# Performance work log

Hardware: AMD Instinct MI355X
Metric: run time of the kernel (lower is better)

## Reference

```python
import jax, jax.numpy as jnp
import numpy as np

N, P, C, K = 1024, 64, 64, 16
C_MID, C_OUT = 128, 128


def setup_inputs() -> dict:
    key = jax.random.key(0)
    k1, k2, k3, k4 = jax.random.split(key, 4)
    x = jax.random.normal(k1, (N, P, C), dtype=jnp.float32)
    mask = jnp.zeros((N, P), dtype=bool)  # True = padded particle
    # Conv2d(2C -> C_MID, 1x1, no bias); Conv2d(C_MID -> C_OUT, 1x1, no bias)
    W1 = jax.random.normal(k2, (C_MID, 2 * C), dtype=jnp.float32) * 0.05
    W2 = jax.random.normal(k3, (C_OUT, C_MID), dtype=jnp.float32) * 0.05
    # Conv1d(C -> C_OUT, kernel 1, no bias) residual path
    Wres = jax.random.normal(k4, (C_OUT, C), dtype=jnp.float32) * 0.05
    return {"x": x, "mask": mask, "W1": W1, "W2": W2, "Wres": Wres}


def reference(x, mask, W1, W2, Wres):
    n, p, c = x.shape
    k = K
    # residual: Conv1d kernel-1 == per-particle matmul  (N,P,C)->(N,P,C_OUT)
    x_res = jnp.einsum('npc,oc->npo', x, Wres)
    # direction = x with padded rows set to +inf (mask all False here)
    direction = jnp.where(mask[..., None], jnp.inf, x)
    # pairwise L2 distance over channel dim: (N,P,P)
    diff = direction[:, :, None, :] - direction[:, None, :, :]
    dist = jnp.sqrt(jnp.sum(diff * diff, axis=-1))
    # smallest K+1 distances, drop self
    _, idx = jax.lax.top_k(-dist, k + 1)
    knn = idx[..., 1:]  # (N,P,K)
    # faithful to torch: gather along the CHANNEL dim with particle indices
    f_center = jnp.broadcast_to(x[:, :, None, :], (n, p, k, c))  # (N,P,K,C)
    f_neighbor = jnp.take_along_axis(f_center, knn[..., None], axis=-1)  # (N,P,K,1)
    feat = jnp.concatenate([f_center, f_center - f_neighbor], axis=-1)  # (N,P,K,2C)
    # 1x1 conv MLP (channels-last layout)
    h = jax.nn.relu(jnp.einsum('npkc,oc->npko', feat, W1))
    h = jax.nn.relu(jnp.einsum('npkc,oc->npko', h, W2))  # (N,P,K,C_OUT)
    # mask neighbors pointing at padded slots, masked mean over K
    n_valid = p - jnp.sum(mask, axis=-1)  # (N,)
    mask_K = knn >= n_valid[:, None, None]  # (N,P,K) bool
    h = jnp.where(mask_K[..., None], 0.0, h)
    denom = (k - jnp.sum(mask_K, axis=-1)).astype(h.dtype)  # (N,P)
    agg = jnp.sum(h, axis=2) / denom[..., None]  # (N,P,C_OUT)
    return jax.nn.relu(agg + x_res)
```

## Files before the change

### kernel.cpp

```cpp
#include <hip/hip_runtime.h>
#include <hip/hip_bf16.h>

typedef __bf16 bf16x8 __attribute__((ext_vector_type(8)));
typedef float  f32x4  __attribute__((ext_vector_type(4)));
typedef unsigned long long u64;

#define MFMA_BF16 __builtin_amdgcn_mfma_f32_16x16x32_bf16

#define WS_W2P  (1u << 20)
#define WS_WCP  ((1u << 20) + 32768u)
#define WS_SSUM ((1u << 20) + 65536u)

#define K1_XS   0
#define K1_SD   17408
#define K1_SQ   34048
#define K1_LDS  38144

__global__ __launch_bounds__(256, 3)
void knn_kernel(const float* __restrict__ x, const float* __restrict__ W1,
                const float* __restrict__ W2, const float* __restrict__ Wres,
                unsigned* __restrict__ ws)
{
    __shared__ char smem[K1_LDS];
    float*    xs   = (float*)(smem + K1_XS);
    float*    sd_t = (float*)(smem + K1_SD);
    unsigned* sqp  = (unsigned*)(smem + K1_SQ);

    const int tid = threadIdx.x;
    const int n   = blockIdx.x;
    const float* __restrict__ xn = x + (size_t)n * 4096;

    #pragma unroll
    for (int i = 0; i < 4; ++i) {
        int e4 = tid + 256 * i;
        f32x4 v = *(const f32x4*)(xn + e4 * 4);
        int row = e4 >> 4, col = (e4 & 15) * 4;
        float* dst = xs + row * 68 + col;
        dst[0] = v[0]; dst[1] = v[1]; dst[2] = v[2]; dst[3] = v[3];
    }
    __syncthreads();

    {
#pragma clang fp contract(off)
        const int p = tid >> 2, rb = tid & 3;
        f32x4 xp4[16];
        const f32x4* xprow = (const f32x4*)(xs + p * 68);
        #pragma unroll
        for (int v = 0; v < 16; ++v) xp4[v] = xprow[v];
        u64 keys[16];
        #pragma unroll
        for (int i = 0; i < 16; ++i) {
            const int q = 4 * i + rb;
            const f32x4* xq4 = (const f32x4*)(xs + q * 68);
            f32x4 d0 = xp4[0] - xq4[0];
            f32x4 d1 = xp4[1] - xq4[1];
            f32x4 rA = d0 * d0;
            f32x4 rB = d1 * d1;
            #pragma unroll
            for (int b = 1; b < 8; ++b) {
                f32x4 e0 = xp4[2*b]   - xq4[2*b];   rA = rA + e0 * e0;
                f32x4 e1 = xp4[2*b+1] - xq4[2*b+1]; rB = rB + e1 * e1;
            }
            float d2 = ((rA[0]+rA[1]) + (rA[2]+rA[3])) + ((rB[0]+rB[1]) + (rB[2]+rB[3]));
            float key = sqrtf(d2);
            unsigned kb = __float_as_uint(key);
            if (q == p) kb = 0x7f800000u;
            keys[i] = ((u64)kb << 8) | (unsigned)q;
        }
        #pragma unroll
        for (int pp = 1; pp < 16; pp <<= 1) {
            #pragma unroll
            for (int k = pp; k >= 1; k >>= 1) {
                #pragma unroll
                for (int j = k & (pp - 1); j + k < 16; j += 2 * k) {
                    #pragma unroll
                    for (int i = 0; i < k; ++i) {
                        if (i + j + k < 16 && ((i + j) / (2 * pp) == (i + j + k) / (2 * pp))) {
                            u64 a = keys[i + j], b = keys[i + j + k];
                            u64 lo = a < b ? a : b;
                            u64 hi = a < b ? b : a;
                            keys[i + j] = lo; keys[i + j + k] = hi;
                        }
                    }
                }
            }
        }
        #pragma unroll
        for (int t = 0; t < 4; ++t) {
            unsigned wq = 0;
            #pragma unroll
            for (int b = 0; b < 4; ++b) {
                int s = 4 * t + b;
                sd_t[(rb * 16 + s) * 65 + p] = __uint_as_float((unsigned)(keys[s] >> 8));
                wq |= ((unsigned)(keys[s] & 0x3fu)) << (8 * b);
            }
            sqp[(rb * 4 + t) * 64 + p] = wq;
        }
    }
    __syncthreads();

    if (tid < 64) {
        const int p = tid;
        float dh[4]; unsigned qh[4]; int ix[4];
        #pragma unroll
        for (int b = 0; b < 4; ++b) {
            ix[b] = 0;
            dh[b] = sd_t[(b * 16) * 65 + p];
            qh[b] = sqp[(b * 4) * 64 + p] & 63u;
        }
        unsigned knacc[4] = {0u, 0u, 0u, 0u};
        for (int s = 0; s < 16; ++s) {
            int bsel = 0; float bd = dh[0]; unsigned bq = qh[0];
            #pragma unroll
            for (int b = 1; b < 4; ++b) {
                bool t = (dh[b] < bd) || (dh[b] == bd && qh[b] < bq);
                if (t) { bd = dh[b]; bq = qh[b]; bsel = b; }
            }
            knacc[s >> 2] |= bq << ((s & 3) * 8);
            int ni = ix[bsel] + 1; ix[bsel] = ni;
            int nc = ni < 15 ? ni : 15;
            float nd = sd_t[(bsel * 16 + nc) * 65 + p];
            unsigned nw = sqp[(bsel * 4 + (nc >> 2)) * 64 + p];
            unsigned nq = (nw >> ((nc & 3) * 8)) & 63u;
            if (ni > 15) nd = __builtin_inff();
            dh[bsel] = nd; qh[bsel] = nq;
        }
        *(uint4*)(ws + (size_t)n * 256 + p * 4) =
            make_uint4(knacc[0], knacc[1], knacc[2], knacc[3]);
    }

    if (n < 32) {
        if (tid < 64) {
            const int l = tid, f = n;
            int ntl = f >> 2, kt = f & 3;
            int o = ntl * 16 + (l & 15);
            int c = kt * 32 + (l >> 4) * 8;
            const float* s0 = W2 + o * 128 + c;
            f32x4 a0 = *(const f32x4*)s0, a1 = *(const f32x4*)(s0 + 4);
            bf16x8 fr;
            fr[0]=(__bf16)a0[0]; fr[1]=(__bf16)a0[1]; fr[2]=(__bf16)a0[2]; fr[3]=(__bf16)a0[3];
            fr[4]=(__bf16)a1[0]; fr[5]=(__bf16)a1[1]; fr[6]=(__bf16)a1[2]; fr[7]=(__bf16)a1[3];
            *(bf16x8*)((__bf16*)((char*)ws + WS_W2P) + (size_t)(f * 64 + l) * 8) = fr;
        }
    } else if (n < 64) {
        if (tid < 64) {
            const int l = tid, f = n - 32;
            int wv = f >> 3, rem = f & 7, ntl = rem >> 1, kt = rem & 1;
            int o = wv * 64 + ntl * 16 + (l & 15);
            int c = kt * 32 + (l >> 4) * 8;
            float v[8];
            if (o < 128) {
                const float* s0 = W1 + o * 128 + c;
                f32x4 a0 = *(const f32x4*)s0,      a1 = *(const f32x4*)(s0 + 4);
                f32x4 b0 = *(const f32x4*)(s0+64), b1 = *(const f32x4*)(s0 + 68);
                v[0]=a0[0]+b0[0]; v[1]=a0[1]+b0[1]; v[2]=a0[2]+b0[2]; v[3]=a0[3]+b0[3];
                v[4]=a1[0]+b1[0]; v[5]=a1[1]+b1[1]; v[6]=a1[2]+b1[2]; v[7]=a1[3]+b1[3];
            } else {
                const float* s0 = Wres + (o - 128) * 64 + c;
                f32x4 a0 = *(const f32x4*)s0, a1 = *(const f32x4*)(s0 + 4);
                v[0]=a0[0]; v[1]=a0[1]; v[2]=a0[2]; v[3]=a0[3];
                v[4]=a1[0]; v[5]=a1[1]; v[6]=a1[2]; v[7]=a1[3];
            }
            bf16x8 fr;
            #pragma unroll
            for (int j = 0; j < 8; ++j) fr[j] = (__bf16)v[j];
            *(bf16x8*)((__bf16*)((char*)ws + WS_WCP) + (size_t)(f * 64 + l) * 8) = fr;
        }
    } else if (n == 64) {
        if (tid < 128) {
            const f32x4* src = (const f32x4*)(W1 + tid * 128 + 64);
            f32x4 a = {0.f, 0.f, 0.f, 0.f};
            #pragma unroll
            for (int i = 0; i < 16; ++i) a += src[i];
            ((float*)((char*)ws + WS_SSUM))[tid] = a[0] + a[1] + a[2] + a[3];
        }
    }
}

#define K2_UB   0
#define K2_XR   32768
#define K2_SS   65536
#define K2_LDS  66048

__global__ __launch_bounds__(256, 2)
void gemm_kernel(const float* __restrict__ x, const unsigned* __restrict__ ws,
                 float* __restrict__ out)
{
    __shared__ char smem[K2_LDS];
    __bf16*   ub   = (__bf16*)(smem + K2_UB);
    __bf16*   xres = (__bf16*)(smem + K2_XR);
    float*    Ssum = (float*)(smem + K2_SS);

    const __bf16* __restrict__ w2p   = (const __bf16*)((const char*)ws + WS_W2P);
    const __bf16* __restrict__ wcp   = (const __bf16*)((const char*)ws + WS_WCP);
    const float*  __restrict__ ssums = (const float*)((const char*)ws + WS_SSUM);

    const int tid  = threadIdx.x;
    const int lane = tid & 63;
    const int w    = tid >> 6;
    const int lm   = lane & 15;
    const int lq   = lane >> 4;
    const int n0   = blockIdx.x * 2;

    if (tid < 128) Ssum[tid] = ssums[tid];

    {
        bf16x8 wcf[4][2];
        #pragma unroll
        for (int ntl = 0; ntl < 4; ++ntl) {
            #pragma unroll
            for (int kt = 0; kt < 2; ++kt)
                wcf[ntl][kt] = *(const bf16x8*)(wcp + (size_t)((w * 8 + ntl * 2 + kt) * 64 + lane) * 8);
        }
        #pragma unroll
        for (int ns = 0; ns < 2; ++ns) {
            const float* xn = x + (size_t)(n0 + ns) * 4096;
            __bf16* ubn = ub   + ns * 8192;
            __bf16* xrn = xres + ns * 8192;
            #pragma unroll
            for (int mt = 0; mt < 4; ++mt) {
                bf16x8 af[2];
                #pragma unroll
                for (int kt = 0; kt < 2; ++kt) {
                    const float* arow = xn + (mt * 16 + lm) * 64 + kt * 32 + lq * 8;
                    f32x4 a0 = *(const f32x4*)arow, a1 = *(const f32x4*)(arow + 4);
                    bf16x8 f;
                    f[0]=(__bf16)a0[0]; f[1]=(__bf16)a0[1]; f[2]=(__bf16)a0[2]; f[3]=(__bf16)a0[3];
                    f[4]=(__bf16)a1[0]; f[5]=(__bf16)a1[1]; f[6]=(__bf16)a1[2]; f[7]=(__bf16)a1[3];
                    af[kt] = f;
                }
                #pragma unroll
                for (int ntl = 0; ntl < 4; ++ntl) {
                    f32x4 acc = {0.f, 0.f, 0.f, 0.f};
                    acc = MFMA_BF16(af[0], wcf[ntl][0], acc, 0, 0, 0);
                    acc = MFMA_BF16(af[1], wcf[ntl][1], acc, 0, 0, 0);
                    int o = w * 64 + ntl * 16 + lm;
                    #pragma unroll
                    for (int r = 0; r < 4; ++r) {
                        int p = mt * 16 + lq * 4 + r;
                        if (o < 128) ubn[p * 128 + o] = (__bf16)acc[r];
                        else         xrn[p * 128 + (o - 128)] = (__bf16)acc[r];
                    }
                }
            }
        }
    }
    __syncthreads();

    {
        bf16x8 w2f[8][4];
        #pragma unroll
        for (int ntl = 0; ntl < 8; ++ntl) {
            #pragma unroll
            for (int kt = 0; kt < 4; ++kt)
                w2f[ntl][kt] = *(const bf16x8*)(w2p + (size_t)((ntl * 4 + kt) * 64 + lane) * 8);
        }
        float ss[4][8];
        #pragma unroll
        for (int kt = 0; kt < 4; ++kt) {
            #pragma unroll
            for (int e = 0; e < 8; ++e) ss[kt][e] = Ssum[kt * 32 + lq * 8 + e];
        }
        const int c0 = lq * 32 + lm;

        #pragma unroll 1
        for (int ns = 0; ns < 2; ++ns) {
            const float*    xn  = x + (size_t)(n0 + ns) * 4096;
            const unsigned* kb  = ws + (size_t)(n0 + ns) * 256;
            const __bf16*   ubn = ub   + ns * 8192;
            const __bf16*   xrn = xres + ns * 8192;
            const size_t outbase = (size_t)(n0 + ns) * 8192;

            #pragma unroll 1
            for (int pi = 0; pi < 16; ++pi) {
                const int p = w + pi * 4;
                unsigned jw = kb[p * 4 + (lm >> 2)];
                int   j     = (int)((jw >> ((lm & 3) * 8)) & 63u);
                float sv_p  = xn[p * 64 + j];

                f32x4 acc[8];
                #pragma unroll
                for (int ntl = 0; ntl < 8; ++ntl) acc[ntl] = f32x4{0.f, 0.f, 0.f, 0.f};
                #pragma unroll
                for (int kt = 0; kt < 4; ++kt) {
                    bf16x8 upv = *(const bf16x8*)(ubn + p * 128 + kt * 32 + lq * 8);
                    bf16x8 af;
                    #pragma unroll
                    for (int e = 0; e < 8; ++e) {
                        float h = fmaf(-sv_p, ss[kt][e], (float)upv[e]);
                        af[e] = (__bf16)fmaxf(h, 0.0f);
                    }
                    #pragma unroll
                    for (int ntl = 0; ntl < 8; ++ntl)
                        acc[ntl] = MFMA_BF16(af, w2f[ntl][kt], acc[ntl], 0, 0, 0);
                }
                float part[8];
                #pragma unroll
                for (int ntl = 0; ntl < 8; ++ntl) {
                    part[ntl] = fmaxf(acc[ntl][0], 0.f) + fmaxf(acc[ntl][1], 0.f)
                              + fmaxf(acc[ntl][2], 0.f) + fmaxf(acc[ntl][3], 0.f);
                }
                float s1[4];
                #pragma unroll
                for (int i = 0; i < 4; ++i) {
                    float mine = (lq < 2) ? part[i] : part[4 + i];
                    float thr  = (lq < 2) ? part[4 + i] : part[i];
                    s1[i] = mine + __shfl_xor(thr, 32);
                }
                float r0, r1;
                {
                    float m0 = ((lq & 1) == 0) ? s1[0] : s1[2];
                    float m1 = ((lq & 1) == 0) ? s1[1] : s1[3];
                    float t0 = ((lq & 1) == 0) ? s1[2] : s1[0];
                    float t1 = ((lq & 1) == 0) ? s1[3] : s1[1];
                    r0 = m0 + __shfl_xor(t0, 16);
                    r1 = m1 + __shfl_xor(t1, 16);
                }
                float x0 = (float)xrn[p * 128 + c0];
                float x1 = (float)xrn[p * 128 + c0 + 16];
                out[outbase + p * 128 + c0]      = fmaxf(r0 * 0.0625f + x0, 0.0f);
                out[outbase + p * 128 + c0 + 16] = fmaxf(r1 * 0.0625f + x1, 0.0f);
            }
        }
    }
}

extern "C" void kernel_launch(void* const* d_in, const int* in_sizes, int n_in,
                              void* d_out, int out_size, void* d_ws, size_t ws_size,
                              hipStream_t stream) {
    const float* x    = (const float*)d_in[0];
    const float* W1   = (const float*)d_in[2];
    const float* W2   = (const float*)d_in[3];
    const float* Wres = (const float*)d_in[4];
    float* outp = (float*)d_out;
    unsigned* ws = (unsigned*)d_ws;
    int nblocks = in_sizes[0] / 4096;
    hipLaunchKernelGGL(knn_kernel,  dim3(nblocks), dim3(256), 0, stream,
                       x, W1, W2, Wres, ws);
    hipLaunchKernelGGL(gemm_kernel, dim3(nblocks / 2), dim3(256), 0, stream,
                       x, ws, outp);
}
```

Before: 155.5 us.

## Exploit distance symmetry via shared matrix, prefetch neighbor indices, pack FMA math

```diff
diff --git a/kernel.cpp b/kernel.cpp
--- a/kernel.cpp
+++ b/kernel.cpp
@@ -3,6 +3,7 @@
 
 typedef __bf16 bf16x8 __attribute__((ext_vector_type(8)));
 typedef float  f32x4  __attribute__((ext_vector_type(4)));
+typedef float  f32x2  __attribute__((ext_vector_type(2)));
 typedef unsigned long long u64;
 
 #define MFMA_BF16 __builtin_amdgcn_mfma_f32_16x16x32_bf16
@@ -23,6 +24,7 @@
 {
     __shared__ char smem[K1_LDS];
     float*    xs   = (float*)(smem + K1_XS);
+    float*    D    = (float*)(smem + K1_SD);
     float*    sd_t = (float*)(smem + K1_SD);
     unsigned* sqp  = (unsigned*)(smem + K1_SQ);
 
@@ -47,26 +49,43 @@
         const f32x4* xprow = (const f32x4*)(xs + p * 68);
         #pragma unroll
         for (int v = 0; v < 16; ++v) xp4[v] = xprow[v];
+
+        const int d0 = (rb - p) & 3;
+        #pragma unroll
+        for (int t = 0; t < 8; ++t) {
+            int delta = (d0 == 0) ? (4 + 4 * t) : (d0 + 4 * t);
+            int q = (p + delta) & 63;
+            bool doit = !(delta == 32 && p >= 32);
+            if (doit) {
+                const f32x4* xq4 = (const f32x4*)(xs + q * 68);
+                f32x4 e0 = xp4[0] - xq4[0];
+                f32x4 e1 = xp4[1] - xq4[1];
+                f32x4 rA = e0 * e0;
+                f32x4 rB = e1 * e1;
+                #pragma unroll
+                for (int b = 1; b < 8; ++b) {
+                    f32x4 g0 = xp4[2*b]   - xq4[2*b];   rA = rA + g0 * g0;
+                    f32x4 g1 = xp4[2*b+1] - xq4[2*b+1]; rB = rB + g1 * g1;
+                }
+                float d2 = ((rA[0]+rA[1]) + (rA[2]+rA[3])) + ((rB[0]+rB[1]) + (rB[2]+rB[3]));
+                D[p * 65 + q] = d2;
+                D[q * 65 + p] = d2;
+            }
+        }
+        __syncthreads();
+
         u64 keys[16];
         #pragma unroll
         for (int i = 0; i < 16; ++i) {
-            const int q = 4 * i + rb;
-            const f32x4* xq4 = (const f32x4*)(xs + q * 68);
-            f32x4 d0 = xp4[0] - xq4[0];
-            f32x4 d1 = xp4[1] - xq4[1];
-            f32x4 rA = d0 * d0;
-            f32x4 rB = d1 * d1;
-            #pragma unroll
-            for (int b = 1; b < 8; ++b) {
-                f32x4 e0 = xp4[2*b]   - xq4[2*b];   rA = rA + e0 * e0;
-                f32x4 e1 = xp4[2*b+1] - xq4[2*b+1]; rB = rB + e1 * e1;
-            }
-            float d2 = ((rA[0]+rA[1]) + (rA[2]+rA[3])) + ((rB[0]+rB[1]) + (rB[2]+rB[3]));
+            int q = 4 * i + rb;
+            float d2  = D[p * 65 + q];
             float key = sqrtf(d2);
             unsigned kb = __float_as_uint(key);
             if (q == p) kb = 0x7f800000u;
             keys[i] = ((u64)kb << 8) | (unsigned)q;
         }
+        __syncthreads();
+
         #pragma unroll
         for (int pp = 1; pp < 16; pp <<= 1) {
             #pragma unroll
@@ -255,13 +274,17 @@
             for (int kt = 0; kt < 4; ++kt)
                 w2f[ntl][kt] = *(const bf16x8*)(w2p + (size_t)((ntl * 4 + kt) * 64 + lane) * 8);
         }
-        float ss[4][8];
+        f32x2 ss2[4][4];
         #pragma unroll
         for (int kt = 0; kt < 4; ++kt) {
             #pragma unroll
-            for (int e = 0; e < 8; ++e) ss[kt][e] = Ssum[kt * 32 + lq * 8 + e];
+            for (int h = 0; h < 4; ++h) {
+                ss2[kt][h][0] = Ssum[kt * 32 + lq * 8 + 2 * h];
+                ss2[kt][h][1] = Ssum[kt * 32 + lq * 8 + 2 * h + 1];
+            }
         }
         const int c0 = lq * 32 + lm;
+        const int jsh = (lm & 3) * 8, jwi = lm >> 2;
 
         #pragma unroll 1
         for (int ns = 0; ns < 2; ++ns) {
@@ -271,13 +294,21 @@
             const __bf16*   xrn = xres + ns * 8192;
             const size_t outbase = (size_t)(n0 + ns) * 8192;
 
+            unsigned jw_a = kb[w * 4 + jwi];
+            unsigned jw_b = kb[(w + 4) * 4 + jwi];
+            float sv_next = xn[w * 64 + ((jw_a >> jsh) & 63u)];
+
             #pragma unroll 1
             for (int pi = 0; pi < 16; ++pi) {
                 const int p = w + pi * 4;
-                unsigned jw = kb[p * 4 + (lm >> 2)];
-                int   j     = (int)((jw >> ((lm & 3) * 8)) & 63u);
-                float sv_p  = xn[p * 64 + j];
-
+                const float sv_p = sv_next;
+                jw_a = jw_b;
+                if (pi < 15) {
+                    if (pi < 14) jw_b = kb[(w + (pi + 2) * 4) * 4 + jwi];
+                    sv_next = xn[(p + 4) * 64 + ((jw_a >> jsh) & 63u)];
+                }
+
+                const f32x2 sv2 = {sv_p, sv_p};
                 f32x4 acc[8];
                 #pragma unroll
                 for (int ntl = 0; ntl < 8; ++ntl) acc[ntl] = f32x4{0.f, 0.f, 0.f, 0.f};
@@ -286,9 +317,11 @@
                     bf16x8 upv = *(const bf16x8*)(ubn + p * 128 + kt * 32 + lq * 8);
                     bf16x8 af;
                     #pragma unroll
-                    for (int e = 0; e < 8; ++e) {
-                        float h = fmaf(-sv_p, ss[kt][e], (float)upv[e]);
-                        af[e] = (__bf16)fmaxf(h, 0.0f);
+                    for (int h = 0; h < 4; ++h) {
+                        f32x2 u2 = { (float)upv[2*h], (float)upv[2*h+1] };
+                        f32x2 m2 = u2 - sv2 * ss2[kt][h];
+                        af[2*h]   = (__bf16)fmaxf(m2[0], 0.0f);
+                        af[2*h+1] = (__bf16)fmaxf(m2[1], 0.0f);
                     }
                     #pragma unroll
                     for (int ntl = 0; ntl < 8; ++ntl)
```

Measured after the change: 151.8 us. 2.4% less time.
